# Performance work log

Measured on AMD Instinct MI355X. Metric: run time of the kernel, lower is better.

Reference implementation:

```python
import jax, jax.numpy as jnp
import numpy as np

D_MODEL = 1024
N_HEADS = 16
D_HEAD = D_MODEL // N_HEADS
QLEN = 512
MLEN = 512
BATCH = 8


def setup_inputs() -> dict:
    key = jax.random.key(0)
    ks = jax.random.split(key, 12)
    s = 0.02
    inputs = jax.random.normal(ks[0], (QLEN, BATCH, D_MODEL), jnp.float32)
    r = jax.random.normal(ks[1], (QLEN + MLEN, 1, D_MODEL), jnp.float32)
    u = jax.random.normal(ks[2], (N_HEADS, D_HEAD), jnp.float32) * s
    v = jax.random.normal(ks[3], (N_HEADS, D_HEAD), jnp.float32) * s
    mem = jax.random.normal(ks[4], (MLEN, BATCH, D_MODEL), jnp.float32)
    # attention params (Transformer-XL style): fused qkv, r-projection, output proj
    W_qkv = jax.random.normal(ks[5], (D_MODEL, 3 * D_MODEL), jnp.float32) * s
    W_r = jax.random.normal(ks[6], (D_MODEL, D_MODEL), jnp.float32) * s
    W_o = jax.random.normal(ks[7], (D_MODEL, D_MODEL), jnp.float32) * s
    # GRU params: input-hidden and hidden-hidden for gates (r, z, n), torch layout
    W_ih = jax.random.normal(ks[8], (3 * D_MODEL, D_MODEL), jnp.float32) * s
    W_hh = jax.random.normal(ks[9], (3 * D_MODEL, D_MODEL), jnp.float32) * s
    b_ih = jax.random.normal(ks[10], (3 * D_MODEL,), jnp.float32) * s
    b_hh = jax.random.normal(ks[11], (3 * D_MODEL,), jnp.float32) * s
    h0 = jnp.zeros((BATCH, D_MODEL), jnp.float32)
    return dict(inputs=inputs, r=r, u=u, v=v, mem=mem, W_qkv=W_qkv, W_r=W_r,
                W_o=W_o, W_ih=W_ih, W_hh=W_hh, b_ih=b_ih, b_hh=b_hh, h0=h0)


def _rel_shift(x):
    # x: [q, k, b, h] -> Transformer-XL relative shift
    q, k, b, h = x.shape
    zero_pad = jnp.zeros((q, 1, b, h), x.dtype)
    x_padded = jnp.concatenate([zero_pad, x], axis=1)        # [q, k+1, b, h]
    x_padded = x_padded.reshape(k + 1, q, b, h)
    return x_padded[1:].reshape(q, k, b, h)


def _attention(inputs, r, u, v, mem, W_qkv, W_r, W_o):
    qlen, bsz, _ = inputs.shape
    cat = jnp.concatenate([mem, inputs], axis=0)             # [klen, b, d]
    klen = cat.shape[0]
    qkv = cat @ W_qkv                                        # [klen, b, 3d]
    w_head_q, w_head_k, w_head_v = jnp.split(qkv, 3, axis=-1)
    w_head_q = w_head_q[-qlen:]                              # [q, b, d]
    r_head_k = (r[:, 0, :] @ W_r).reshape(klen, N_HEADS, D_HEAD)  # [k, h, dh]

    q_ = w_head_q.reshape(qlen, bsz, N_HEADS, D_HEAD)
    k_ = w_head_k.reshape(klen, bsz, N_HEADS, D_HEAD)
    v_ = w_head_v.reshape(klen, bsz, N_HEADS, D_HEAD)

    AC = jnp.einsum('ibhd,jbhd->ijbh', q_ + u[None, None], k_)
    BD = jnp.einsum('ibhd,jhd->ijbh', q_ + v[None, None], r_head_k)
    BD = _rel_shift(BD)
    scale = 1.0 / np.sqrt(D_HEAD)
    attn_score = (AC + BD) * scale                           # [q, k, b, h]

    # causal mask with memory: query i attends to keys j <= i + mlen
    mlen = klen - qlen
    i = jnp.arange(qlen)[:, None]
    j = jnp.arange(klen)[None, :]
    mask = j > (i + mlen)                                    # [q, k]
    attn_score = jnp.where(mask[:, :, None, None], -jnp.inf, attn_score)

    attn_prob = jax.nn.softmax(attn_score, axis=1)
    attn_vec = jnp.einsum('ijbh,jbhd->ibhd', attn_prob, v_)
    attn_vec = attn_vec.reshape(qlen, bsz, D_MODEL)
    return attn_vec @ W_o                                    # [q, b, d]


def _gru(x, h0, W_ih, W_hh, b_ih, b_hh):
    # x: [T, B, D]; torch GRU cell math
    Wi_r, Wi_z, Wi_n = jnp.split(W_ih, 3, axis=0)
    Wh_r, Wh_z, Wh_n = jnp.split(W_hh, 3, axis=0)
    bi_r, bi_z, bi_n = jnp.split(b_ih, 3)
    bh_r, bh_z, bh_n = jnp.split(b_hh, 3)

    # precompute input projections for all timesteps
    xr = x @ Wi_r.T + bi_r
    xz = x @ Wi_z.T + bi_z
    xn = x @ Wi_n.T + bi_n

    def step(h, xs):
        xr_t, xz_t, xn_t = xs
        r = jax.nn.sigmoid(xr_t + h @ Wh_r.T + bh_r)
        z = jax.nn.sigmoid(xz_t + h @ Wh_z.T + bh_z)
        n = jnp.tanh(xn_t + r * (h @ Wh_n.T + bh_n))
        h_new = (1.0 - z) * n + z * h
        return h_new, h_new

    _, ys = jax.lax.scan(step, h0, (xr, xz, xn))
    return ys                                                # [T, B, D]


def reference(inputs, r, u, v, mem, W_qkv, W_r, W_o, W_ih, W_hh, b_ih, b_hh, h0):
    y = _attention(inputs, r, u, v, mem, W_qkv, W_r, W_o)
    return _gru(y, h0, W_ih, W_hh, b_ih, b_hh)
```

## Files before the change

kernel.cpp:

```cpp
#include <hip/hip_runtime.h>
#include <math.h>


typedef short bf16x8 __attribute__((ext_vector_type(8)));
typedef float f32x4 __attribute__((ext_vector_type(4)));

union FragU { uint4 u; bf16x8 h; };

__device__ inline void split2(float x0, float x1, unsigned& hi, unsigned& lo) {
    unsigned u0 = __float_as_uint(x0), u1 = __float_as_uint(x1);
    float h0 = __uint_as_float(u0 & 0xffff0000u);
    float h1 = __uint_as_float(u1 & 0xffff0000u);
    unsigned l0 = __float_as_uint(x0 - h0), l1 = __float_as_uint(x1 - h1);
    hi = (u0 >> 16) | (u1 & 0xffff0000u);
    lo = (l0 >> 16) | (l1 & 0xffff0000u);
}

__device__ __forceinline__ unsigned long long ld_coh64(const void* p) {
    return __hip_atomic_load((const unsigned long long*)p, __ATOMIC_RELAXED,
                             __HIP_MEMORY_SCOPE_AGENT);
}
__device__ __forceinline__ void st_coh64(void* p, unsigned long long v) {
    __hip_atomic_store((unsigned long long*)p, v, __ATOMIC_RELAXED,
                       __HIP_MEMORY_SCOPE_AGENT);
}

template<bool TR>
__global__ __launch_bounds__(256) void prep_w(
    const float* __restrict__ W, unsigned* __restrict__ out, int Nr, int K, int ldw)
{
    int idx = blockIdx.x * 256 + threadIdx.x;
    int cpr = K >> 3;
    if (idx >= Nr * cpr) return;
    int n, c;
    if (TR) { n = idx % Nr; c = idx / Nr; }
    else    { c = idx % cpr; n = idx / cpr; }
    int kt = c >> 2, j = c & 3;
    int k = kt * 32 + j * 8;
    float x[8];
    #pragma unroll
    for (int i = 0; i < 8; ++i)
        x[i] = TR ? W[(size_t)(k + i) * ldw + n] : W[(size_t)n * ldw + k + i];
    unsigned h[4], l[4];
    split2(x[0], x[1], h[0], l[0]);
    split2(x[2], x[3], h[1], l[1]);
    split2(x[4], x[5], h[2], l[2]);
    split2(x[6], x[7], h[3], l[3]);
    unsigned* base = out + (size_t)n * K + kt * 32;
    *(uint4*)(base + (((2 * j) ^ (n & 7)) * 4))     = make_uint4(h[0], h[1], h[2], h[3]);
    *(uint4*)(base + (((2 * j + 1) ^ (n & 7)) * 4)) = make_uint4(l[0], l[1], l[2], l[3]);
}

template<int AMODE, bool BIAS>
__global__ __launch_bounds__(256) void gemm_mfma(
    const float* __restrict__ A, const float* __restrict__ A2,
    const unsigned* __restrict__ Bp, const float* __restrict__ bias,
    float* __restrict__ C, int M, int N, int K, int lda, int ldc)
{
    __shared__ uint4 Ab[1024];
    __shared__ uint4 Bb[1024];
    int tid = threadIdx.x;
    int lane = tid & 63, wid = tid >> 6;
    int wr = wid >> 1, wc = wid & 1;
    int n0 = blockIdx.x * 128, m0 = blockIdx.y * 128;
    int r15 = lane & 15, s = lane >> 4;

    f32x4 acc[4][4];
    #pragma unroll
    for (int i = 0; i < 4; ++i)
        #pragma unroll
        for (int j = 0; j < 4; ++j) acc[i][j] = 0.0f;

    for (int kt = 0; kt < (K >> 5); ++kt) {
        int k0 = kt * 32;
        #pragma unroll
        for (int q = 0; q < 2; ++q) {
            int idx = q * 256 + tid;
            int row = idx >> 2, j = idx & 3;
            const float* ap;
            if (AMODE == 1) {
                int gm = m0 + row;
                ap = (gm < 4096) ? (A + (size_t)gm * lda) : (A2 + (size_t)(gm - 4096) * lda);
            } else {
                ap = A + (size_t)(m0 + row) * lda;
            }
            float4 x0 = *(const float4*)(ap + k0 + j * 8);
            float4 x1 = *(const float4*)(ap + k0 + j * 8 + 4);
            unsigned h[4], l[4];
            split2(x0.x, x0.y, h[0], l[0]);
            split2(x0.z, x0.w, h[1], l[1]);
            split2(x1.x, x1.y, h[2], l[2]);
            split2(x1.z, x1.w, h[3], l[3]);
            Ab[row * 8 + (((2 * j) ^ (row & 7)))]     = make_uint4(h[0], h[1], h[2], h[3]);
            Ab[row * 8 + (((2 * j + 1) ^ (row & 7)))] = make_uint4(l[0], l[1], l[2], l[3]);
        }
        #pragma unroll
        for (int q = 0; q < 4; ++q) {
            int idx = q * 256 + tid;
            int row = idx >> 3, slot = idx & 7;
            Bb[idx] = *(const uint4*)(Bp + (size_t)(n0 + row) * K + k0 + slot * 4);
        }
        __syncthreads();
        FragU ahi[4], alo[4], bhi[4], blo[4];
        #pragma unroll
        for (int f = 0; f < 4; ++f) {
            int ar = wr * 64 + f * 16 + r15;
            ahi[f].u = Ab[ar * 8 + ((2 * s) ^ (ar & 7))];
            alo[f].u = Ab[ar * 8 + ((2 * s + 1) ^ (ar & 7))];
            int br = wc * 64 + f * 16 + r15;
            bhi[f].u = Bb[br * 8 + ((2 * s) ^ (br & 7))];
            blo[f].u = Bb[br * 8 + ((2 * s + 1) ^ (br & 7))];
        }
        #pragma unroll
        for (int fi = 0; fi < 4; ++fi)
            #pragma unroll
            for (int fj = 0; fj < 4; ++fj) {
                acc[fi][fj] = __builtin_amdgcn_mfma_f32_16x16x32_bf16(ahi[fi].h, bhi[fj].h, acc[fi][fj], 0, 0, 0);
                acc[fi][fj] = __builtin_amdgcn_mfma_f32_16x16x32_bf16(ahi[fi].h, blo[fj].h, acc[fi][fj], 0, 0, 0);
                acc[fi][fj] = __builtin_amdgcn_mfma_f32_16x16x32_bf16(alo[fi].h, bhi[fj].h, acc[fi][fj], 0, 0, 0);
            }
        __syncthreads();
    }
    int r4 = (lane >> 4) * 4;
    #pragma unroll
    for (int fj = 0; fj < 4; ++fj) {
        int n = n0 + wc * 64 + fj * 16 + r15;
        float bv = BIAS ? bias[n] : 0.f;
        #pragma unroll
        for (int fi = 0; fi < 4; ++fi) {
            int m = m0 + wr * 64 + fi * 16 + r4;
            #pragma unroll
            for (int r = 0; r < 4; ++r)
                C[(size_t)(m + r) * ldc + n] = acc[fi][fj][r] + bv;
        }
    }
}

__global__ __launch_bounds__(256) void attn_fused(
    const float* __restrict__ qkv, const float* __restrict__ rk,
    const float* __restrict__ u_, const float* __restrict__ v_,
    float* __restrict__ y1)
{
    __shared__ float qu[64][68], qv[64][68], Kt[64][68], Vt[64][68];
    __shared__ float RKs[128][68];
    __shared__ float S[64][68];
    __shared__ float mrow[64], lrow[64], scalef[64];
    __shared__ float pmax[64][16], psum[64][16];

    int tid = threadIdx.x;
    int it = blockIdx.x, b = blockIdx.y, h = blockIdx.z;
    int i0 = it * 64;
    int ti = tid >> 4, tj = tid & 15;

    {
        int r = tid >> 2, c0 = (tid & 3) * 16;
        size_t base = ((size_t)(i0 + r + 512) * 8 + b) * 3072 + h * 64;
        #pragma unroll
        for (int q = 0; q < 4; ++q) {
            int c = c0 + q * 4;
            float4 qq = *(const float4*)&qkv[base + c];
            float4 uu = *(const float4*)&u_[h * 64 + c];
            float4 vv = *(const float4*)&v_[h * 64 + c];
            *(float4*)&qu[r][c] = make_float4(qq.x + uu.x, qq.y + uu.y, qq.z + uu.z, qq.w + uu.w);
            *(float4*)&qv[r][c] = make_float4(qq.x + vv.x, qq.y + vv.y, qq.z + vv.z, qq.w + vv.w);
        }
    }
    if (tid < 64) { mrow[tid] = -1e30f; lrow[tid] = 0.f; }

    float Od[4][4] = {};
    int njt = it + 9;

    for (int jt = 0; jt < njt; ++jt) {
        int j0 = jt * 64;
        __syncthreads();
        {
            int r = tid >> 2, c0 = (tid & 3) * 16;
            size_t kb = ((size_t)(j0 + r) * 8 + b) * 3072 + 1024 + h * 64;
            #pragma unroll
            for (int q = 0; q < 4; ++q) {
                int c = c0 + q * 4;
                *(float4*)&Kt[r][c] = *(const float4*)&qkv[kb + c];
                *(float4*)&Vt[r][c] = *(const float4*)&qkv[kb + 1024 + c];
            }
        }
        {
            int r2 = tid >> 1, c0 = (tid & 1) * 32;
            int jj = j0 - i0 + 448 + r2;
            jj = jj < 0 ? 0 : (jj > 1023 ? 1023 : jj);
            size_t rb = (size_t)jj * 1024 + h * 64;
            #pragma unroll
            for (int q = 0; q < 8; ++q) {
                int c = c0 + q * 4;
                *(float4*)&RKs[r2][c] = *(const float4*)&rk[rb + c];
            }
        }
        __syncthreads();

        float acc[4][4] = {};
        int jlb = (tj - ti) * 4 + 60;
        #pragma unroll 4
        for (int d4 = 0; d4 < 64; d4 += 4) {
            float4 Aq[4], Cq[4], Kv[4], Rv[7];
            #pragma unroll
            for (int i = 0; i < 4; ++i) {
                Aq[i] = *(float4*)&qu[ti * 4 + i][d4];
                Cq[i] = *(float4*)&qv[ti * 4 + i][d4];
                Kv[i] = *(float4*)&Kt[tj * 4 + i][d4];
            }
            #pragma unroll
            for (int t = 0; t < 7; ++t)
                Rv[t] = *(float4*)&RKs[jlb + t][d4];
            #pragma unroll
            for (int i = 0; i < 4; ++i)
                #pragma unroll
                for (int j = 0; j < 4; ++j) {
                    float4 kk = Kv[j];
                    float4 rr = Rv[j - i + 3];
                    acc[i][j] += Aq[i].x * kk.x + Aq[i].y * kk.y + Aq[i].z * kk.z + Aq[i].w * kk.w
                               + Cq[i].x * rr.x + Cq[i].y * rr.y + Cq[i].z * rr.z + Cq[i].w * rr.w;
                }
        }
        #pragma unroll
        for (int i = 0; i < 4; ++i) {
            int gi = i0 + ti * 4 + i;
            float mx = -1e30f;
            #pragma unroll
            for (int j = 0; j < 4; ++j) {
                int gj = j0 + tj * 4 + j;
                float vS = acc[i][j] * 0.125f;
                if (gj > gi + 512) vS = -1e30f;
                acc[i][j] = vS;
                mx = fmaxf(mx, vS);
            }
            pmax[ti * 4 + i][tj] = mx;
        }
        __syncthreads();
        if (tid < 64) {
            float mo = mrow[tid], mn = mo;
            #pragma unroll
            for (int t = 0; t < 16; ++t) mn = fmaxf(mn, pmax[tid][t]);
            mrow[tid] = mn;
            scalef[tid] = __expf(mo - mn);
        }
        __syncthreads();
        #pragma unroll
        for (int i = 0; i < 4; ++i) {
            int ri = ti * 4 + i;
            float mn = mrow[ri];
            float4 pv;
            pv.x = __expf(acc[i][0] - mn);
            pv.y = __expf(acc[i][1] - mn);
            pv.z = __expf(acc[i][2] - mn);
            pv.w = __expf(acc[i][3] - mn);
            *(float4*)&S[ri][tj * 4] = pv;
            psum[ri][tj] = pv.x + pv.y + pv.z + pv.w;
            float scl = scalef[ri];
            #pragma unroll
            for (int j2 = 0; j2 < 4; ++j2) Od[i][j2] *= scl;
        }
        __syncthreads();
        if (tid < 64) {
            float s = 0.f;
            #pragma unroll
            for (int t = 0; t < 16; ++t) s += psum[tid][t];
            lrow[tid] = lrow[tid] * scalef[tid] + s;
        }
        #pragma unroll 4
        for (int jb = 0; jb < 64; jb += 4) {
            float4 p0 = *(float4*)&S[ti * 4 + 0][jb];
            float4 p1 = *(float4*)&S[ti * 4 + 1][jb];
            float4 p2 = *(float4*)&S[ti * 4 + 2][jb];
            float4 p3 = *(float4*)&S[ti * 4 + 3][jb];
            float4 v0 = *(float4*)&Vt[jb + 0][tj * 4];
            float4 v1 = *(float4*)&Vt[jb + 1][tj * 4];
            float4 v2 = *(float4*)&Vt[jb + 2][tj * 4];
            float4 v3 = *(float4*)&Vt[jb + 3][tj * 4];
            float4 pr[4] = {p0, p1, p2, p3};
            #pragma unroll
            for (int i = 0; i < 4; ++i) {
                Od[i][0] += pr[i].x * v0.x + pr[i].y * v1.x + pr[i].z * v2.x + pr[i].w * v3.x;
                Od[i][1] += pr[i].x * v0.y + pr[i].y * v1.y + pr[i].z * v2.y + pr[i].w * v3.y;
                Od[i][2] += pr[i].x * v0.z + pr[i].y * v1.z + pr[i].z * v2.z + pr[i].w * v3.z;
                Od[i][3] += pr[i].x * v0.w + pr[i].y * v1.w + pr[i].z * v2.w + pr[i].w * v3.w;
            }
        }
    }
    __syncthreads();
    #pragma unroll
    for (int i = 0; i < 4; ++i) {
        int ri = ti * 4 + i;
        float inv = 1.f / lrow[ri];
        float4 o = make_float4(Od[i][0] * inv, Od[i][1] * inv, Od[i][2] * inv, Od[i][3] * inv);
        *(float4*)&y1[((size_t)(i0 + ri) * 8 + b) * 1024 + h * 64 + tj * 4] = o;
    }
}

__global__ __launch_bounds__(256) void prep_whh(
    const float* __restrict__ Whh, uint4* __restrict__ outp)
{
    int idx = blockIdx.x * 256 + threadIdx.x;
    if (idx >= 393216) return;
    int lane = idx & 63;
    int rest = idx >> 6;
    int gate = rest % 3;
    int kt   = (rest / 3) & 31;
    int g64  = rest / 96;
    int n = gate * 1024 + g64 * 16 + (lane & 15);
    int k = kt * 32 + (lane >> 4) * 8;
    const float* src = Whh + (size_t)n * 1024 + k;
    float4 x0 = *(const float4*)src, x1 = *(const float4*)(src + 4);
    unsigned h[4], l[4];
    split2(x0.x, x0.y, h[0], l[0]);
    split2(x0.z, x0.w, h[1], l[1]);
    split2(x1.x, x1.y, h[2], l[2]);
    split2(x1.z, x1.w, h[3], l[3]);
    outp[((size_t)rest * 2 + 0) * 64 + lane] = make_uint4(h[0], h[1], h[2], h[3]);
    outp[((size_t)rest * 2 + 1) * 64 + lane] = make_uint4(l[0], l[1], l[2], l[3]);
}

__global__ __launch_bounds__(256, 1) void gru_persist2(
    const float* __restrict__ h0, float* __restrict__ hA, float* __restrict__ hB,
    const uint4* __restrict__ WhhG, const float* __restrict__ bhh,
    const float* __restrict__ xg, float* __restrict__ out,
    unsigned* __restrict__ flags)
{
    __shared__ uint4 Bf[4096];
    __shared__ float red[3][64][4];
    int tid = threadIdx.x;
    int lane = tid & 63, wv = tid >> 6;
    int g64 = blockIdx.x;

    int col = lane & 15;
    int d0 = g64 * 16 + (lane >> 4) * 4;
    bool act = (wv == 0) && (col < 8);
    float4 br4 = make_float4(0, 0, 0, 0), bz4 = br4, bn4 = br4;
    if (act) {
        br4 = *(const float4*)&bhh[d0];
        bz4 = *(const float4*)&bhh[1024 + d0];
        bn4 = *(const float4*)&bhh[2048 + d0];
    }
    const uint4* wb = WhhG + (size_t)g64 * 12288 + (wv < 3 ? wv : 0) * 128 + lane;

    for (int t = 0; t < 512; ++t) {
        const float* hi_ = (t == 0) ? h0 : ((t & 1) ? hA : hB);
        float* ho = (t & 1) ? hB : hA;

        float4 xr4, xz4, xn4;
        unsigned long long hp01 = 0, hp23 = 0;
        if (act) {
            size_t xb = ((size_t)t * 8 + col) * 3072 + d0;
            xr4 = *(const float4*)&xg[xb];
            xz4 = *(const float4*)&xg[xb + 1024];
            xn4 = *(const float4*)&xg[xb + 2048];
            hp01 = ld_coh64(hi_ + col * 1024 + d0);
            hp23 = ld_coh64(hi_ + col * 1024 + d0 + 2);
        }

        uint4 wA[16], wB[16];
        #pragma unroll
        for (int q = 0; q < 8; ++q) {
            wA[2 * q]     = wb[q * 384];
            wA[2 * q + 1] = wb[q * 384 + 64];
        }

        unsigned long long hq[16];
        #pragma unroll
        for (int i = 0; i < 4; ++i) {
            int s = i * 256 + tid;
            const float* hp = hi_ + (s & 7) * 1024 + (s >> 5) * 32 + ((s >> 3) & 3) * 8;
            #pragma unroll
            for (int q = 0; q < 4; ++q) hq[i * 4 + q] = ld_coh64(hp + q * 2);
        }
        #pragma unroll
        for (int i = 0; i < 4; ++i) {
            int s = i * 256 + tid;
            int b = s & 7, oct = (s >> 3) & 3, kt = s >> 5;
            float x[8];
            #pragma unroll
            for (int q = 0; q < 4; ++q) {
                x[2 * q]     = __uint_as_float((unsigned)(hq[i * 4 + q] & 0xffffffffu));
                x[2 * q + 1] = __uint_as_float((unsigned)(hq[i * 4 + q] >> 32));
            }
            unsigned hh[4], ll[4];
            split2(x[0], x[1], hh[0], ll[0]);
            split2(x[2], x[3], hh[1], ll[1]);
            split2(x[4], x[5], hh[2], ll[2]);
            split2(x[6], x[7], hh[3], ll[3]);
            int ln = oct * 16 + b;
            Bf[(kt * 2 + 0) * 64 + ln] = make_uint4(hh[0], hh[1], hh[2], hh[3]);
            Bf[(kt * 2 + 1) * 64 + ln] = make_uint4(ll[0], ll[1], ll[2], ll[3]);
        }
        __syncthreads();

        f32x4 acc = 0.0f;
        #define GRU_LOAD(dst, c0)                                   \
            _Pragma("unroll")                                       \
            for (int q = 0; q < 8; ++q) {                           \
                dst[2 * q]     = wb[((c0) * 8 + q) * 384];          \
                dst[2 * q + 1] = wb[((c0) * 8 + q) * 384 + 64];     \
            }
        #define GRU_COMP(src, c0)                                   \
            _Pragma("unroll")                                       \
            for (int q = 0; q < 8; ++q) {                           \
                int kt = (c0) * 8 + q;                              \
                FragU ah, al, bh, bl;                               \
                ah.u = src[2 * q]; al.u = src[2 * q + 1];           \
                bh.u = Bf[(kt * 2 + 0) * 64 + lane];                \
                bl.u = Bf[(kt * 2 + 1) * 64 + lane];                \
                acc = __builtin_amdgcn_mfma_f32_16x16x32_bf16(ah.h, bh.h, acc, 0, 0, 0); \
                acc = __builtin_amdgcn_mfma_f32_16x16x32_bf16(ah.h, bl.h, acc, 0, 0, 0); \
                acc = __builtin_amdgcn_mfma_f32_16x16x32_bf16(al.h, bh.h, acc, 0, 0, 0); \
            }
        if (wv < 3) {
            GRU_LOAD(wB, 1);
            GRU_COMP(wA, 0);
            GRU_LOAD(wA, 2);
            GRU_COMP(wB, 1);
            GRU_LOAD(wB, 3);
            GRU_COMP(wA, 2);
            GRU_COMP(wB, 3);
            *(f32x4*)&red[wv][lane][0] = acc;
        }
        #undef GRU_LOAD
        #undef GRU_COMP
        __syncthreads();

        if (act) {
            f32x4 aR = *(f32x4*)&red[0][lane][0];
            f32x4 aZ = *(f32x4*)&red[1][lane][0];
            f32x4 aN = *(f32x4*)&red[2][lane][0];
            float xr[4] = {xr4.x, xr4.y, xr4.z, xr4.w};
            float xz[4] = {xz4.x, xz4.y, xz4.z, xz4.w};
            float xn[4] = {xn4.x, xn4.y, xn4.z, xn4.w};
            float hp[4] = {__uint_as_float((unsigned)(hp01 & 0xffffffffu)),
                           __uint_as_float((unsigned)(hp01 >> 32)),
                           __uint_as_float((unsigned)(hp23 & 0xffffffffu)),
                           __uint_as_float((unsigned)(hp23 >> 32))};
            float br[4] = {br4.x, br4.y, br4.z, br4.w};
            float bz[4] = {bz4.x, bz4.y, bz4.z, bz4.w};
            float bn[4] = {bn4.x, bn4.y, bn4.z, bn4.w};
            float hn[4];
            #pragma unroll
            for (int r = 0; r < 4; ++r) {
                float rr = 1.f / (1.f + __expf(-(xr[r] + aR[r] + br[r])));
                float zz = 1.f / (1.f + __expf(-(xz[r] + aZ[r] + bz[r])));
                float nn = tanhf(xn[r] + rr * (aN[r] + bn[r]));
                hn[r] = (1.f - zz) * nn + zz * hp[r];
            }
            unsigned long long v01 = (unsigned long long)__float_as_uint(hn[0])
                                   | ((unsigned long long)__float_as_uint(hn[1]) << 32);
            unsigned long long v23 = (unsigned long long)__float_as_uint(hn[2])
                                   | ((unsigned long long)__float_as_uint(hn[3]) << 32);
            st_coh64(ho + col * 1024 + d0, v01);
            st_coh64(ho + col * 1024 + d0 + 2, v23);
            *(float4*)&out[((size_t)t * 8 + col) * 1024 + d0] =
                make_float4(hn[0], hn[1], hn[2], hn[3]);
        }

        if (t != 511) {
            __syncthreads();
            unsigned tgt = (unsigned)t + 1u;
            if (tid < 64) {
                if (tid == 0)
                    __hip_atomic_store(&flags[(size_t)g64 * 16], tgt,
                                       __ATOMIC_RELAXED, __HIP_MEMORY_SCOPE_AGENT);
                const unsigned* fp = &flags[(size_t)tid * 16];
                for (;;) {
                    unsigned f = __hip_atomic_load(fp, __ATOMIC_RELAXED,
                                                   __HIP_MEMORY_SCOPE_AGENT);
                    if (__all(f >= tgt)) break;
                }
            }
            __syncthreads();
        }
    }
}

__global__ __launch_bounds__(192, 1) void gru_step_mfma(
    const float* __restrict__ hin, float* __restrict__ hout,
    const uint4* __restrict__ WhhG, const float* __restrict__ bhh,
    const float* __restrict__ xg, float* __restrict__ out, int t)
{
    __shared__ uint4 Bf[4096];
    __shared__ float red[3][64][4];
    int tid = threadIdx.x;
    int lane = tid & 63, wv = tid >> 6;
    int g64 = blockIdx.x;

    int col = lane & 15;
    int d0 = g64 * 16 + (lane >> 4) * 4;
    bool act = (wv == 0) && (col < 8);
    float4 xr4, xz4, xn4, hp4, br4, bz4, bn4;
    if (act) {
        size_t xb = ((size_t)t * 8 + col) * 3072 + d0;
        xr4 = *(const float4*)&xg[xb];
        xz4 = *(const float4*)&xg[xb + 1024];
        xn4 = *(const float4*)&xg[xb + 2048];
        hp4 = *(const float4*)&hin[col * 1024 + d0];
        br4 = *(const float4*)&bhh[d0];
        bz4 = *(const float4*)&bhh[1024 + d0];
        bn4 = *(const float4*)&bhh[2048 + d0];
    }

    const uint4* wb = WhhG + (size_t)g64 * 12288 + wv * 128 + lane;
    uint4 wA[16], wB[16];
    #pragma unroll
// ... 66 lines not shown
            float rr = 1.f / (1.f + __expf(-(xr[r] + aR[r] + br[r])));
            float zz = 1.f / (1.f + __expf(-(xz[r] + aZ[r] + bz[r])));
            float nn = tanhf(xn[r] + rr * (aN[r] + bn[r]));
            hn[r] = (1.f - zz) * nn + zz * hp[r];
        }
        float4 hv = make_float4(hn[0], hn[1], hn[2], hn[3]);
        *(float4*)&hout[col * 1024 + d0] = hv;
        *(float4*)&out[((size_t)t * 8 + col) * 1024 + d0] = hv;
    }
}

extern "C" void kernel_launch(void* const* d_in, const int* in_sizes, int n_in,
                              void* d_out, int out_size, void* d_ws, size_t ws_size,
                              hipStream_t stream) {
    (void)in_sizes; (void)n_in; (void)out_size; (void)ws_size;
    const float* inputs = (const float*)d_in[0];
    const float* r_in   = (const float*)d_in[1];
    const float* u_in   = (const float*)d_in[2];
    const float* v_in   = (const float*)d_in[3];
    const float* mem    = (const float*)d_in[4];
    const float* Wqkv   = (const float*)d_in[5];
    const float* Wr     = (const float*)d_in[6];
    const float* Wo     = (const float*)d_in[7];
    const float* Wih    = (const float*)d_in[8];
    const float* Whh    = (const float*)d_in[9];
    const float* bih    = (const float*)d_in[10];
    const float* bhh    = (const float*)d_in[11];
    const float* h0     = (const float*)d_in[12];
    float* out = (float*)d_out;
    float* ws = (float*)d_ws;

    float*    qkv   = ws;
    float*    rk    = ws + 25165824;
    float*    y1    = ws + 26214400;
    float*    y2    = ws + 30408704;
    float*    xg    = ws + 34603008;
    float*    hA    = ws + 47185920;
    float*    hB    = ws + 47194112;
    unsigned* WqkvP = (unsigned*)(ws + 47202304);
    unsigned* WrP   = (unsigned*)(ws + 50348032);
    unsigned* WoP   = (unsigned*)(ws + 51396608);
    unsigned* WihP  = (unsigned*)(ws + 52445184);
    unsigned* flags = (unsigned*)(ws + 55590912);
    uint4*    WhhG  = (uint4*)qkv;

    dim3 blk(256);
    prep_w<true ><<<1536, blk, 0, stream>>>(Wqkv, WqkvP, 3072, 1024, 3072);
    prep_w<true ><<< 512, blk, 0, stream>>>(Wr,   WrP,   1024, 1024, 1024);
    prep_w<true ><<< 512, blk, 0, stream>>>(Wo,   WoP,   1024, 1024, 1024);
    prep_w<false><<<1536, blk, 0, stream>>>(Wih,  WihP,  3072, 1024, 1024);
    hipMemsetAsync(flags, 0, 4096, stream);

    gemm_mfma<1, false><<<dim3(24, 64), blk, 0, stream>>>(
        mem, inputs, WqkvP, nullptr, qkv, 8192, 3072, 1024, 1024, 3072);
    gemm_mfma<0, false><<<dim3(8, 8), blk, 0, stream>>>(
        r_in, nullptr, WrP, nullptr, rk, 1024, 1024, 1024, 1024, 1024);
    attn_fused<<<dim3(8, 8, 16), blk, 0, stream>>>(qkv, rk, u_in, v_in, y1);
    prep_whh<<<1536, blk, 0, stream>>>(Whh, WhhG);
    gemm_mfma<0, false><<<dim3(8, 32), blk, 0, stream>>>(
        y1, nullptr, WoP, nullptr, y2, 4096, 1024, 1024, 1024, 1024);
    gemm_mfma<0, true><<<dim3(24, 32), blk, 0, stream>>>(
        y2, nullptr, WihP, bih, xg, 4096, 3072, 1024, 1024, 3072);

    {
        const float* a0 = h0; float* a1 = hA; float* a2 = hB;
        const uint4* a3 = WhhG; const float* a4 = bhh; const float* a5 = xg;
        float* a6 = out; unsigned* a7 = flags;
        void* args[8] = {&a0, &a1, &a2, &a3, &a4, &a5, &a6, &a7};
        hipError_t e = hipLaunchCooperativeKernel((void*)gru_persist2,
                                                  dim3(64), dim3(256), args, 0, stream);
        if (e != hipSuccess) {
            const float* hin = h0;
            for (int s = 0; s < 512; ++s) {
                float* hp = (s & 1) ? hB : hA;
                gru_step_mfma<<<64, dim3(192), 0, stream>>>(hin, hp, WhhG, bhh, xg, out, s);
                hin = hp;
            }
        }
    }
}
```

Baseline: 4.737 ms.

## Replace global barrier in persistent GRU with per-slice flag waits

The all-block barrier at the end of each GRU timestep is replaced by fine-grained waits: each thread spins only on the flag of the block that produced the h slice it is about to load. The flag is published right after the h store drains (s_waitcnt vmcnt(0)), before the output write. The previous hidden state is kept in registers instead of being reloaded, and the MFMA chain is split into four independent accumulators to shorten the dependency chain. Blocks can now start a step as soon as their inputs are ready, but this relies on relaxed atomics plus a waitcnt for ordering and has more threads spinning on flags.

```diff
diff --git a/kernel.cpp b/kernel.cpp
--- a/kernel.cpp
+++ b/kernel.cpp
@@ -318,7 +318,7 @@
     outp[((size_t)rest * 2 + 1) * 64 + lane] = make_uint4(l[0], l[1], l[2], l[3]);
 }
 
-__global__ __launch_bounds__(256, 1) void gru_persist2(
+__global__ __launch_bounds__(256, 1) void gru_persist3(
     const float* __restrict__ h0, float* __restrict__ hA, float* __restrict__ hB,
     const uint4* __restrict__ WhhG, const float* __restrict__ bhh,
     const float* __restrict__ xg, float* __restrict__ out,
@@ -333,48 +333,62 @@
     int col = lane & 15;
     int d0 = g64 * 16 + (lane >> 4) * 4;
     bool act = (wv == 0) && (col < 8);
-    float4 br4 = make_float4(0, 0, 0, 0), bz4 = br4, bn4 = br4;
+    float4 br4 = make_float4(0, 0, 0, 0), bz4 = br4, bn4 = br4, hprev4 = br4;
     if (act) {
         br4 = *(const float4*)&bhh[d0];
         bz4 = *(const float4*)&bhh[1024 + d0];
         bn4 = *(const float4*)&bhh[2048 + d0];
+        hprev4 = *(const float4*)&h0[col * 1024 + d0];
     }
     const uint4* wb = WhhG + (size_t)g64 * 12288 + (wv < 3 ? wv : 0) * 128 + lane;
+
+    int toff[4], tkt[4], tln[4];
+    const unsigned* tfl[4];
+    #pragma unroll
+    for (int i = 0; i < 4; ++i) {
+        int s = i * 256 + tid;
+        int b = s & 7, oct = (s >> 3) & 3, kt = s >> 5;
+        toff[i] = b * 1024 + kt * 32 + oct * 8;
+        tkt[i] = kt;
+        tln[i] = oct * 16 + b;
+        tfl[i] = &flags[(size_t)(2 * kt + (oct >> 1)) * 16];
+    }
 
     for (int t = 0; t < 512; ++t) {
         const float* hi_ = (t == 0) ? h0 : ((t & 1) ? hA : hB);
         float* ho = (t & 1) ? hB : hA;
 
         float4 xr4, xz4, xn4;
-        unsigned long long hp01 = 0, hp23 = 0;
         if (act) {
             size_t xb = ((size_t)t * 8 + col) * 3072 + d0;
             xr4 = *(const float4*)&xg[xb];
             xz4 = *(const float4*)&xg[xb + 1024];
             xn4 = *(const float4*)&xg[xb + 2048];
-            hp01 = ld_coh64(hi_ + col * 1024 + d0);
-            hp23 = ld_coh64(hi_ + col * 1024 + d0 + 2);
         }
 
         uint4 wA[16], wB[16];
-        #pragma unroll
-        for (int q = 0; q < 8; ++q) {
-            wA[2 * q]     = wb[q * 384];
-            wA[2 * q + 1] = wb[q * 384 + 64];
+        if (wv < 3) {
+            #pragma unroll
+            for (int q = 0; q < 8; ++q) {
+                wA[2 * q]     = wb[q * 384];
+                wA[2 * q + 1] = wb[q * 384 + 64];
+            }
         }
 
         unsigned long long hq[16];
+        unsigned tgt = (unsigned)t;
         #pragma unroll
         for (int i = 0; i < 4; ++i) {
-            int s = i * 256 + tid;
-            const float* hp = hi_ + (s & 7) * 1024 + (s >> 5) * 32 + ((s >> 3) & 3) * 8;
+            if (t > 0) {
+                while (__hip_atomic_load(tfl[i], __ATOMIC_RELAXED,
+                                         __HIP_MEMORY_SCOPE_AGENT) < tgt) {}
+            }
+            const float* hp = hi_ + toff[i];
             #pragma unroll
             for (int q = 0; q < 4; ++q) hq[i * 4 + q] = ld_coh64(hp + q * 2);
         }
         #pragma unroll
         for (int i = 0; i < 4; ++i) {
-            int s = i * 256 + tid;
-            int b = s & 7, oct = (s >> 3) & 3, kt = s >> 5;
             float x[8];
             #pragma unroll
             for (int q = 0; q < 4; ++q) {
@@ -386,20 +400,18 @@
             split2(x[2], x[3], hh[1], ll[1]);
             split2(x[4], x[5], hh[2], ll[2]);
             split2(x[6], x[7], hh[3], ll[3]);
-            int ln = oct * 16 + b;
-            Bf[(kt * 2 + 0) * 64 + ln] = make_uint4(hh[0], hh[1], hh[2], hh[3]);
-            Bf[(kt * 2 + 1) * 64 + ln] = make_uint4(ll[0], ll[1], ll[2], ll[3]);
-        }
-        __syncthreads();
-
-        f32x4 acc = 0.0f;
+            Bf[(tkt[i] * 2 + 0) * 64 + tln[i]] = make_uint4(hh[0], hh[1], hh[2], hh[3]);
+            Bf[(tkt[i] * 2 + 1) * 64 + tln[i]] = make_uint4(ll[0], ll[1], ll[2], ll[3]);
+        }
+        __syncthreads();
+
         #define GRU_LOAD(dst, c0)                                   \
             _Pragma("unroll")                                       \
             for (int q = 0; q < 8; ++q) {                           \
                 dst[2 * q]     = wb[((c0) * 8 + q) * 384];          \
                 dst[2 * q + 1] = wb[((c0) * 8 + q) * 384 + 64];     \
             }
-        #define GRU_COMP(src, c0)                                   \
+        #define GRU_COMP(src, c0, a)                                \
             _Pragma("unroll")                                       \
             for (int q = 0; q < 8; ++q) {                           \
                 int kt = (c0) * 8 + q;                              \
@@ -407,24 +419,27 @@
                 ah.u = src[2 * q]; al.u = src[2 * q + 1];           \
                 bh.u = Bf[(kt * 2 + 0) * 64 + lane];                \
                 bl.u = Bf[(kt * 2 + 1) * 64 + lane];                \
-                acc = __builtin_amdgcn_mfma_f32_16x16x32_bf16(ah.h, bh.h, acc, 0, 0, 0); \
-                acc = __builtin_amdgcn_mfma_f32_16x16x32_bf16(ah.h, bl.h, acc, 0, 0, 0); \
-                acc = __builtin_amdgcn_mfma_f32_16x16x32_bf16(al.h, bh.h, acc, 0, 0, 0); \
+                a = __builtin_amdgcn_mfma_f32_16x16x32_bf16(ah.h, bh.h, a, 0, 0, 0); \
+                a = __builtin_amdgcn_mfma_f32_16x16x32_bf16(ah.h, bl.h, a, 0, 0, 0); \
+                a = __builtin_amdgcn_mfma_f32_16x16x32_bf16(al.h, bh.h, a, 0, 0, 0); \
             }
         if (wv < 3) {
+            f32x4 a0 = 0.0f, a1 = 0.0f, a2 = 0.0f, a3 = 0.0f;
             GRU_LOAD(wB, 1);
-            GRU_COMP(wA, 0);
+            GRU_COMP(wA, 0, a0);
             GRU_LOAD(wA, 2);
-            GRU_COMP(wB, 1);
+            GRU_COMP(wB, 1, a1);
             GRU_LOAD(wB, 3);
-            GRU_COMP(wA, 2);
-            GRU_COMP(wB, 3);
-            *(f32x4*)&red[wv][lane][0] = acc;
+            GRU_COMP(wA, 2, a2);
+            GRU_COMP(wB, 3, a3);
+            f32x4 av = (a0 + a1) + (a2 + a3);
+            *(f32x4*)&red[wv][lane][0] = av;
         }
         #undef GRU_LOAD
         #undef GRU_COMP
         __syncthreads();
 
+        float hn[4];
         if (act) {
             f32x4 aR = *(f32x4*)&red[0][lane][0];
             f32x4 aZ = *(f32x4*)&red[1][lane][0];
@@ -432,14 +447,10 @@
             float xr[4] = {xr4.x, xr4.y, xr4.z, xr4.w};
             float xz[4] = {xz4.x, xz4.y, xz4.z, xz4.w};
             float xn[4] = {xn4.x, xn4.y, xn4.z, xn4.w};
-            float hp[4] = {__uint_as_float((unsigned)(hp01 & 0xffffffffu)),
-                           __uint_as_float((unsigned)(hp01 >> 32)),
-                           __uint_as_float((unsigned)(hp23 & 0xffffffffu)),
-                           __uint_as_float((unsigned)(hp23 >> 32))};
+            float hp[4] = {hprev4.x, hprev4.y, hprev4.z, hprev4.w};
             float br[4] = {br4.x, br4.y, br4.z, br4.w};
             float bz[4] = {bz4.x, bz4.y, bz4.z, bz4.w};
             float bn[4] = {bn4.x, bn4.y, bn4.z, bn4.w};
-            float hn[4];
             #pragma unroll
             for (int r = 0; r < 4; ++r) {
                 float rr = 1.f / (1.f + __expf(-(xr[r] + aR[r] + br[r])));
@@ -453,25 +464,18 @@
                                    | ((unsigned long long)__float_as_uint(hn[3]) << 32);
             st_coh64(ho + col * 1024 + d0, v01);
             st_coh64(ho + col * 1024 + d0 + 2, v23);
+        }
+        if (wv == 0) {
+            asm volatile("s_waitcnt vmcnt(0)" ::: "memory");
+            __builtin_amdgcn_sched_barrier(0);
+            if (tid == 0 && t != 511)
+                __hip_atomic_store(&flags[(size_t)g64 * 16], (unsigned)(t + 1),
+                                   __ATOMIC_RELAXED, __HIP_MEMORY_SCOPE_AGENT);
+        }
+        if (act) {
             *(float4*)&out[((size_t)t * 8 + col) * 1024 + d0] =
                 make_float4(hn[0], hn[1], hn[2], hn[3]);
-        }
-
-        if (t != 511) {
-            __syncthreads();
-            unsigned tgt = (unsigned)t + 1u;
-            if (tid < 64) {
-                if (tid == 0)
-                    __hip_atomic_store(&flags[(size_t)g64 * 16], tgt,
-                                       __ATOMIC_RELAXED, __HIP_MEMORY_SCOPE_AGENT);
-                const unsigned* fp = &flags[(size_t)tid * 16];
-                for (;;) {
-                    unsigned f = __hip_atomic_load(fp, __ATOMIC_RELAXED,
-                                                   __HIP_MEMORY_SCOPE_AGENT);
-                    if (__all(f >= tgt)) break;
-                }
-            }
-            __syncthreads();
+            hprev4 = make_float4(hn[0], hn[1], hn[2], hn[3]);
         }
     }
 }
@@ -639,7 +643,7 @@
         const uint4* a3 = WhhG; const float* a4 = bhh; const float* a5 = xg;
         float* a6 = out; unsigned* a7 = flags;
         void* args[8] = {&a0, &a1, &a2, &a3, &a4, &a5, &a6, &a7};
-        hipError_t e = hipLaunchCooperativeKernel((void*)gru_persist2,
+        hipError_t e = hipLaunchCooperativeKernel((void*)gru_persist3,
                                                   dim3(64), dim3(256), args, 0, stream);
         if (e != hipSuccess) {
             const float* hin = h0;
```

Measured after the change: 4.827 ms. No clear change (+1.9%).

## Pre-split GEMM A operands to bf16 hi/lo layout and load via global_load_lds

Applied to the files above, without the earlier changes.

Adds a prep pass that splits the concatenated mem/inputs, y1 and y2 activations into swizzled bf16 hi/lo packed layout. A new gemm_pp kernel then streams both A and B tiles straight into LDS with global_load_lds instead of converting fp32 inside the GEMM. This removes the per-tile split work and register staging from the GEMM inner loop. In exchange it adds extra prep kernels and global traffic, and reuses workspace regions (qkv, xg) as scratch, which relies on their lifetimes not overlapping.

```diff
diff --git a/kernel.cpp b/kernel.cpp
--- a/kernel.cpp
+++ b/kernel.cpp
@@ -23,6 +23,12 @@
 __device__ __forceinline__ void st_coh64(void* p, unsigned long long v) {
     __hip_atomic_store((unsigned long long*)p, v, __ATOMIC_RELAXED,
                        __HIP_MEMORY_SCOPE_AGENT);
+}
+
+__device__ __forceinline__ void gl_lds16(const uint4* g, uint4* l) {
+    __builtin_amdgcn_global_load_lds(
+        (const __attribute__((address_space(1))) uint4*)g,
+        (__attribute__((address_space(3))) uint4*)l, 16, 0, 0);
 }
 
 template<bool TR>
@@ -51,6 +57,93 @@
     *(uint4*)(base + (((2 * j + 1) ^ (n & 7)) * 4)) = make_uint4(l[0], l[1], l[2], l[3]);
 }
 
+__global__ __launch_bounds__(256) void prep_cat(
+    const float* __restrict__ mem, const float* __restrict__ inputs,
+    unsigned* __restrict__ out)
+{
+    int idx = blockIdx.x * 256 + threadIdx.x;
+    if (idx >= 1048576) return;
+    int c = idx & 127, n = idx >> 7;
+    int kt = c >> 2, j = c & 3;
+    int k = kt * 32 + j * 8;
+    const float* src = (n < 4096) ? (mem + (size_t)n * 1024 + k)
+                                  : (inputs + (size_t)(n - 4096) * 1024 + k);
+    float4 x0 = *(const float4*)src, x1 = *(const float4*)(src + 4);
+    unsigned h[4], l[4];
+    split2(x0.x, x0.y, h[0], l[0]);
+    split2(x0.z, x0.w, h[1], l[1]);
+    split2(x1.x, x1.y, h[2], l[2]);
+    split2(x1.z, x1.w, h[3], l[3]);
+    unsigned* base = out + (size_t)n * 1024 + kt * 32;
+    *(uint4*)(base + (((2 * j) ^ (n & 7)) * 4))     = make_uint4(h[0], h[1], h[2], h[3]);
+    *(uint4*)(base + (((2 * j + 1) ^ (n & 7)) * 4)) = make_uint4(l[0], l[1], l[2], l[3]);
+}
+
+template<bool BIAS>
+__global__ __launch_bounds__(256) void gemm_pp(
+    const uint4* __restrict__ Ap4, const uint4* __restrict__ Bp4,
+    const float* __restrict__ bias, float* __restrict__ C, int K, int ldc)
+{
+    __shared__ uint4 Ab[1024];
+    __shared__ uint4 Bb[1024];
+    int tid = threadIdx.x;
+    int lane = tid & 63, wid = tid >> 6;
+    int wr = wid >> 1, wc = wid & 1;
+    int n0 = blockIdx.x * 128, m0 = blockIdx.y * 128;
+    int r15 = lane & 15, s = lane >> 4;
+    int K4 = K >> 2;
+
+    f32x4 acc[4][4];
+    #pragma unroll
+    for (int i = 0; i < 4; ++i)
+        #pragma unroll
+        for (int j = 0; j < 4; ++j) acc[i][j] = 0.0f;
+
+    for (int kt = 0; kt < (K >> 5); ++kt) {
+        #pragma unroll
+        for (int q = 0; q < 4; ++q) {
+            int base = q * 256 + wid * 64;
+            int idx  = base + lane;
+            int row = idx >> 3, slot = idx & 7;
+            gl_lds16(Ap4 + (size_t)(m0 + row) * K4 + kt * 8 + slot, &Ab[base]);
+            gl_lds16(Bp4 + (size_t)(n0 + row) * K4 + kt * 8 + slot, &Bb[base]);
+        }
+        __syncthreads();
+        FragU ahi[4], alo[4], bhi[4], blo[4];
+        #pragma unroll
+        for (int f = 0; f < 4; ++f) {
+            int ar = wr * 64 + f * 16 + r15;
+            ahi[f].u = Ab[ar * 8 + ((2 * s) ^ (ar & 7))];
+            alo[f].u = Ab[ar * 8 + ((2 * s + 1) ^ (ar & 7))];
+            int br = wc * 64 + f * 16 + r15;
+            bhi[f].u = Bb[br * 8 + ((2 * s) ^ (br & 7))];
+            blo[f].u = Bb[br * 8 + ((2 * s + 1) ^ (br & 7))];
+        }
+        #pragma unroll
+        for (int fi = 0; fi < 4; ++fi)
+            #pragma unroll
+            for (int fj = 0; fj < 4; ++fj) {
+                acc[fi][fj] = __builtin_amdgcn_mfma_f32_16x16x32_bf16(ahi[fi].h, bhi[fj].h, acc[fi][fj], 0, 0, 0);
+                acc[fi][fj] = __builtin_amdgcn_mfma_f32_16x16x32_bf16(ahi[fi].h, blo[fj].h, acc[fi][fj], 0, 0, 0);
+                acc[fi][fj] = __builtin_amdgcn_mfma_f32_16x16x32_bf16(alo[fi].h, bhi[fj].h, acc[fi][fj], 0, 0, 0);
+            }
+        __syncthreads();
+    }
+    int r4 = (lane >> 4) * 4;
+    #pragma unroll
+    for (int fj = 0; fj < 4; ++fj) {
+        int n = n0 + wc * 64 + fj * 16 + r15;
+        float bv = BIAS ? bias[n] : 0.f;
+        #pragma unroll
+        for (int fi = 0; fi < 4; ++fi) {
+            int m = m0 + wr * 64 + fi * 16 + r4;
+            #pragma unroll
+            for (int r = 0; r < 4; ++r)
+                C[(size_t)(m + r) * ldc + n] = acc[fi][fj][r] + bv;
+        }
+    }
+}
+
 template<int AMODE, bool BIAS>
 __global__ __launch_bounds__(256) void gemm_mfma(
     const float* __restrict__ A, const float* __restrict__ A2,
@@ -615,6 +708,9 @@
     unsigned* WihP  = (unsigned*)(ws + 52445184);
     unsigned* flags = (unsigned*)(ws + 55590912);
     uint4*    WhhG  = (uint4*)qkv;
+    unsigned* y1P   = (unsigned*)(qkv + 4194304);
+    unsigned* y2P   = (unsigned*)(qkv + 8388608);
+    unsigned* catP  = (unsigned*)xg;
 
     dim3 blk(256);
     prep_w<true ><<<1536, blk, 0, stream>>>(Wqkv, WqkvP, 3072, 1024, 3072);
@@ -623,16 +719,19 @@
     prep_w<false><<<1536, blk, 0, stream>>>(Wih,  WihP,  3072, 1024, 1024);
     hipMemsetAsync(flags, 0, 4096, stream);
 
-    gemm_mfma<1, false><<<dim3(24, 64), blk, 0, stream>>>(
-        mem, inputs, WqkvP, nullptr, qkv, 8192, 3072, 1024, 1024, 3072);
+    prep_cat<<<4096, blk, 0, stream>>>(mem, inputs, catP);
+    gemm_pp<false><<<dim3(24, 64), blk, 0, stream>>>(
+        (const uint4*)catP, (const uint4*)WqkvP, nullptr, qkv, 1024, 3072);
     gemm_mfma<0, false><<<dim3(8, 8), blk, 0, stream>>>(
         r_in, nullptr, WrP, nullptr, rk, 1024, 1024, 1024, 1024, 1024);
     attn_fused<<<dim3(8, 8, 16), blk, 0, stream>>>(qkv, rk, u_in, v_in, y1);
     prep_whh<<<1536, blk, 0, stream>>>(Whh, WhhG);
-    gemm_mfma<0, false><<<dim3(8, 32), blk, 0, stream>>>(
-        y1, nullptr, WoP, nullptr, y2, 4096, 1024, 1024, 1024, 1024);
-    gemm_mfma<0, true><<<dim3(24, 32), blk, 0, stream>>>(
-        y2, nullptr, WihP, bih, xg, 4096, 3072, 1024, 1024, 3072);
+    prep_w<false><<<2048, blk, 0, stream>>>(y1, y1P, 4096, 1024, 1024);
+    gemm_pp<false><<<dim3(8, 32), blk, 0, stream>>>(
+        (const uint4*)y1P, (const uint4*)WoP, nullptr, y2, 1024, 1024);
+    prep_w<false><<<2048, blk, 0, stream>>>(y2, y2P, 4096, 1024, 1024);
+    gemm_pp<true><<<dim3(24, 32), blk, 0, stream>>>(
+        (const uint4*)y2P, (const uint4*)WihP, bih, xg, 1024, 3072);
 
     {
         const float* a0 = h0; float* a1 = hA; float* a2 = hB;
```

Result: no change. 4.719 ms (-0.4%).

## Pre-split GEMM operands to bf16 hi/lo and load tiles via global_load_lds

Applied to the files above, without the earlier changes.

Merges all weight and activation preparation into one prep_all kernel that writes operands in the swizzled bf16 hi/lo layout. The GEMMs then stream both A and B tiles straight into LDS with global_load_lds instead of splitting A inside the inner loop. The QKV GEMM skips the Q columns for memory rows, since only the last qlen rows of Q are used. The attention and W_o GEMM epilogues now emit the split-packed layout for the next GEMM. Attention softmax row max and sum move from shared-memory reductions with barriers to wave shuffles. The cost is more kernels writing packed intermediates and reuse of the xg buffer as scratch.

```diff
diff --git a/kernel.cpp b/kernel.cpp
--- a/kernel.cpp
+++ b/kernel.cpp
@@ -25,22 +25,15 @@
                        __HIP_MEMORY_SCOPE_AGENT);
 }
 
-template<bool TR>
-__global__ __launch_bounds__(256) void prep_w(
-    const float* __restrict__ W, unsigned* __restrict__ out, int Nr, int K, int ldw)
+__device__ __forceinline__ void gl_lds16(const uint4* g, uint4* l) {
+    __builtin_amdgcn_global_load_lds(
+        (const __attribute__((address_space(1))) uint4*)g,
+        (__attribute__((address_space(3))) uint4*)l, 16, 0, 0);
+}
+
+__device__ __forceinline__ void split_store8(
+    const float* x, unsigned* out, int n, int K, int kt, int j)
 {
-    int idx = blockIdx.x * 256 + threadIdx.x;
-    int cpr = K >> 3;
-    if (idx >= Nr * cpr) return;
-    int n, c;
-    if (TR) { n = idx % Nr; c = idx / Nr; }
-    else    { c = idx % cpr; n = idx / cpr; }
-    int kt = c >> 2, j = c & 3;
-    int k = kt * 32 + j * 8;
-    float x[8];
-    #pragma unroll
-    for (int i = 0; i < 8; ++i)
-        x[i] = TR ? W[(size_t)(k + i) * ldw + n] : W[(size_t)n * ldw + k + i];
     unsigned h[4], l[4];
     split2(x[0], x[1], h[0], l[0]);
     split2(x[2], x[3], h[1], l[1]);
@@ -51,19 +44,72 @@
     *(uint4*)(base + (((2 * j + 1) ^ (n & 7)) * 4)) = make_uint4(l[0], l[1], l[2], l[3]);
 }
 
-template<int AMODE, bool BIAS>
-__global__ __launch_bounds__(256) void gemm_mfma(
-    const float* __restrict__ A, const float* __restrict__ A2,
-    const unsigned* __restrict__ Bp, const float* __restrict__ bias,
-    float* __restrict__ C, int M, int N, int K, int lda, int ldc)
+#define SEG0 1048576
+#define SEG1 1441792
+#define SEG2 1572864
+#define SEG3 1703936
+#define SEG4 2097152
+#define SEG5 2228224
+
+__global__ __launch_bounds__(256) void prep_all(
+    const float* __restrict__ mem, const float* __restrict__ inputs,
+    const float* __restrict__ Wqkv, const float* __restrict__ Wr,
+    const float* __restrict__ Wo, const float* __restrict__ Wih,
+    const float* __restrict__ r_in,
+    unsigned* __restrict__ catP, unsigned* __restrict__ WqkvP,
+    unsigned* __restrict__ WrP, unsigned* __restrict__ WoP,
+    unsigned* __restrict__ WihP, unsigned* __restrict__ rP)
 {
-    __shared__ uint4 Ab[1024];
-    __shared__ uint4 Bb[1024];
+    int idx = blockIdx.x * 256 + threadIdx.x;
+    if (idx >= SEG5) return;
+    float x[8];
+    if (idx < SEG0) {
+        int c = idx & 127, n = idx >> 7;
+        int kt = c >> 2, j = c & 3, k = kt * 32 + j * 8;
+        const float* src = (n < 4096) ? (mem + (size_t)n * 1024 + k)
+                                      : (inputs + (size_t)(n - 4096) * 1024 + k);
+        float4 a = *(const float4*)src, b = *(const float4*)(src + 4);
+        x[0]=a.x; x[1]=a.y; x[2]=a.z; x[3]=a.w; x[4]=b.x; x[5]=b.y; x[6]=b.z; x[7]=b.w;
+        split_store8(x, catP, n, 1024, kt, j);
+    } else if (idx < SEG3) {
+        int i, Nr, ldw; const float* W; unsigned* out;
+        if (idx < SEG1)      { i = idx - SEG0; Nr = 3072; ldw = 3072; W = Wqkv; out = WqkvP; }
+        else if (idx < SEG2) { i = idx - SEG1; Nr = 1024; ldw = 1024; W = Wr;   out = WrP;  }
+        else                 { i = idx - SEG2; Nr = 1024; ldw = 1024; W = Wo;   out = WoP;  }
+        int n = i % Nr, c = i / Nr;
+        int kt = c >> 2, j = c & 3, k = kt * 32 + j * 8;
+        #pragma unroll
+        for (int q = 0; q < 8; ++q) x[q] = W[(size_t)(k + q) * ldw + n];
+        split_store8(x, out, n, 1024, kt, j);
+    } else {
+        int i; const float* W; unsigned* out;
+        if (idx < SEG4) { i = idx - SEG3; W = Wih;  out = WihP; }
+        else            { i = idx - SEG4; W = r_in; out = rP;   }
+        int c = i & 127, n = i >> 7;
+        int kt = c >> 2, j = c & 3, k = kt * 32 + j * 8;
+        float4 a = *(const float4*)(W + (size_t)n * 1024 + k);
+        float4 b = *(const float4*)(W + (size_t)n * 1024 + k + 4);
+        x[0]=a.x; x[1]=a.y; x[2]=a.z; x[3]=a.w; x[4]=b.x; x[5]=b.y; x[6]=b.z; x[7]=b.w;
+        split_store8(x, out, n, 1024, kt, j);
+    }
+}
+
+template<bool BIAS, bool SPLITOUT>
+__global__ __launch_bounds__(256) void gemm_pp(
+    const uint4* __restrict__ Ap4, const uint4* __restrict__ Bp4,
+    const float* __restrict__ bias, float* __restrict__ C,
+    unsigned* __restrict__ Cp, int K, int ldc)
+{
+    __shared__ uint4 SH[2048];
+    uint4* Ab = SH;
+    uint4* Bb = SH + 1024;
     int tid = threadIdx.x;
     int lane = tid & 63, wid = tid >> 6;
     int wr = wid >> 1, wc = wid & 1;
     int n0 = blockIdx.x * 128, m0 = blockIdx.y * 128;
     int r15 = lane & 15, s = lane >> 4;
+    int r4 = (lane >> 4) * 4;
+    int K4 = K >> 2;
 
     f32x4 acc[4][4];
     #pragma unroll
@@ -72,33 +118,13 @@
         for (int j = 0; j < 4; ++j) acc[i][j] = 0.0f;
 
     for (int kt = 0; kt < (K >> 5); ++kt) {
-        int k0 = kt * 32;
-        #pragma unroll
-        for (int q = 0; q < 2; ++q) {
-            int idx = q * 256 + tid;
-            int row = idx >> 2, j = idx & 3;
-            const float* ap;
-            if (AMODE == 1) {
-                int gm = m0 + row;
-                ap = (gm < 4096) ? (A + (size_t)gm * lda) : (A2 + (size_t)(gm - 4096) * lda);
-            } else {
-                ap = A + (size_t)(m0 + row) * lda;
-            }
-            float4 x0 = *(const float4*)(ap + k0 + j * 8);
-            float4 x1 = *(const float4*)(ap + k0 + j * 8 + 4);
-            unsigned h[4], l[4];
-            split2(x0.x, x0.y, h[0], l[0]);
-            split2(x0.z, x0.w, h[1], l[1]);
-            split2(x1.x, x1.y, h[2], l[2]);
-            split2(x1.z, x1.w, h[3], l[3]);
-            Ab[row * 8 + (((2 * j) ^ (row & 7)))]     = make_uint4(h[0], h[1], h[2], h[3]);
-            Ab[row * 8 + (((2 * j + 1) ^ (row & 7)))] = make_uint4(l[0], l[1], l[2], l[3]);
-        }
         #pragma unroll
         for (int q = 0; q < 4; ++q) {
-            int idx = q * 256 + tid;
+            int base = q * 256 + wid * 64;
+            int idx  = base + lane;
             int row = idx >> 3, slot = idx & 7;
-            Bb[idx] = *(const uint4*)(Bp + (size_t)(n0 + row) * K + k0 + slot * 4);
+            gl_lds16(Ap4 + (size_t)(m0 + row) * K4 + kt * 8 + slot, &Ab[base]);
+            gl_lds16(Bp4 + (size_t)(n0 + row) * K4 + kt * 8 + slot, &Bb[base]);
         }
         __syncthreads();
         FragU ahi[4], alo[4], bhi[4], blo[4];
@@ -121,17 +147,46 @@
             }
         __syncthreads();
     }
-    int r4 = (lane >> 4) * 4;
-    #pragma unroll
-    for (int fj = 0; fj < 4; ++fj) {
-        int n = n0 + wc * 64 + fj * 16 + r15;
-        float bv = BIAS ? bias[n] : 0.f;
-        #pragma unroll
-        for (int fi = 0; fi < 4; ++fi) {
-            int m = m0 + wr * 64 + fi * 16 + r4;
-            #pragma unroll
-            for (int r = 0; r < 4; ++r)
-                C[(size_t)(m + r) * ldc + n] = acc[fi][fj][r] + bv;
+
+    if (!SPLITOUT) {
+        #pragma unroll
+        for (int fj = 0; fj < 4; ++fj) {
+            int n = n0 + wc * 64 + fj * 16 + r15;
+            float bv = BIAS ? bias[n] : 0.f;
+            #pragma unroll
+            for (int fi = 0; fi < 4; ++fi) {
+                int m = m0 + wr * 64 + fi * 16 + r4;
+                #pragma unroll
+                for (int r = 0; r < 4; ++r)
+                    C[(size_t)(m + r) * ldc + n] = acc[fi][fj][r] + bv;
+            }
+        }
+    } else {
+        float* Cs = (float*)SH;
+        #pragma unroll
+        for (int half = 0; half < 2; ++half) {
+            __syncthreads();
+            if (wr == half) {
+                #pragma unroll
+                for (int fi = 0; fi < 4; ++fi)
+                    #pragma unroll
+                    for (int fj = 0; fj < 4; ++fj)
+                        #pragma unroll
+                        for (int r = 0; r < 4; ++r)
+                            Cs[(fi * 16 + r4 + r) * 128 + wc * 64 + fj * 16 + r15] = acc[fi][fj][r];
+            }
+            __syncthreads();
+            #pragma unroll
+            for (int q = 0; q < 4; ++q) {
+                int oc = q * 256 + tid;
+                int lr = oc >> 4, oct = oc & 15;
+                float x[8];
+                *(float4*)&x[0] = *(float4*)&Cs[lr * 128 + oct * 8];
+                *(float4*)&x[4] = *(float4*)&Cs[lr * 128 + oct * 8 + 4];
+                int m = m0 + half * 64 + lr;
+                int k = n0 + oct * 8;
+                split_store8(x, Cp, m, ldc, k >> 5, (k >> 3) & 3);
+            }
         }
     }
 }
@@ -139,13 +194,11 @@
 __global__ __launch_bounds__(256) void attn_fused(
     const float* __restrict__ qkv, const float* __restrict__ rk,
     const float* __restrict__ u_, const float* __restrict__ v_,
-    float* __restrict__ y1)
+    unsigned* __restrict__ y1P)
 {
     __shared__ float qu[64][68], qv[64][68], Kt[64][68], Vt[64][68];
     __shared__ float RKs[128][68];
     __shared__ float S[64][68];
-    __shared__ float mrow[64], lrow[64], scalef[64];
-    __shared__ float pmax[64][16], psum[64][16];
 
     int tid = threadIdx.x;
     int it = blockIdx.x, b = blockIdx.y, h = blockIdx.z;
@@ -165,8 +218,9 @@
             *(float4*)&qv[r][c] = make_float4(qq.x + vv.x, qq.y + vv.y, qq.z + vv.z, qq.w + vv.w);
         }
     }
-    if (tid < 64) { mrow[tid] = -1e30f; lrow[tid] = 0.f; }
-
+
+    float m[4] = {-1e30f, -1e30f, -1e30f, -1e30f};
+    float l[4] = {0.f, 0.f, 0.f, 0.f};
     float Od[4][4] = {};
     int njt = it + 9;
 
@@ -232,39 +286,29 @@
                 acc[i][j] = vS;
                 mx = fmaxf(mx, vS);
             }
-            pmax[ti * 4 + i][tj] = mx;
-        }
-        __syncthreads();
-        if (tid < 64) {
-            float mo = mrow[tid], mn = mo;
-            #pragma unroll
-            for (int t = 0; t < 16; ++t) mn = fmaxf(mn, pmax[tid][t]);
-            mrow[tid] = mn;
-            scalef[tid] = __expf(mo - mn);
-        }
-        __syncthreads();
-        #pragma unroll
-        for (int i = 0; i < 4; ++i) {
-            int ri = ti * 4 + i;
-            float mn = mrow[ri];
+            mx = fmaxf(mx, __shfl_xor(mx, 1));
+            mx = fmaxf(mx, __shfl_xor(mx, 2));
+            mx = fmaxf(mx, __shfl_xor(mx, 4));
+            mx = fmaxf(mx, __shfl_xor(mx, 8));
+            float mn = fmaxf(m[i], mx);
+            float sc = __expf(m[i] - mn);
+            m[i] = mn;
             float4 pv;
             pv.x = __expf(acc[i][0] - mn);
             pv.y = __expf(acc[i][1] - mn);
             pv.z = __expf(acc[i][2] - mn);
             pv.w = __expf(acc[i][3] - mn);
-            *(float4*)&S[ri][tj * 4] = pv;
-            psum[ri][tj] = pv.x + pv.y + pv.z + pv.w;
-            float scl = scalef[ri];
-            #pragma unroll
-            for (int j2 = 0; j2 < 4; ++j2) Od[i][j2] *= scl;
-        }
-        __syncthreads();
-        if (tid < 64) {
-            float s = 0.f;
-            #pragma unroll
-            for (int t = 0; t < 16; ++t) s += psum[tid][t];
-            lrow[tid] = lrow[tid] * scalef[tid] + s;
-        }
+            *(float4*)&S[ti * 4 + i][tj * 4] = pv;
+            float ps = pv.x + pv.y + pv.z + pv.w;
+            ps += __shfl_xor(ps, 1);
+            ps += __shfl_xor(ps, 2);
+            ps += __shfl_xor(ps, 4);
+            ps += __shfl_xor(ps, 8);
+            l[i] = l[i] * sc + ps;
+            #pragma unroll
+            for (int j2 = 0; j2 < 4; ++j2) Od[i][j2] *= sc;
+        }
+        asm volatile("" ::: "memory");
         #pragma unroll 4
         for (int jb = 0; jb < 64; jb += 4) {
             float4 p0 = *(float4*)&S[ti * 4 + 0][jb];
@@ -285,13 +329,21 @@
             }
         }
     }
-    __syncthreads();
     #pragma unroll
     for (int i = 0; i < 4; ++i) {
         int ri = ti * 4 + i;
-        float inv = 1.f / lrow[ri];
+        float inv = 1.f / l[i];
         float4 o = make_float4(Od[i][0] * inv, Od[i][1] * inv, Od[i][2] * inv, Od[i][3] * inv);
-        *(float4*)&y1[((size_t)(i0 + ri) * 8 + b) * 1024 + h * 64 + tj * 4] = o;
+        int n = (i0 + ri) * 8 + b;
+        unsigned hw0, hw1, lw0, lw1;
+        split2(o.x, o.y, hw0, lw0);
+        split2(o.z, o.w, hw1, lw1);
+        int kt2 = 2 * h + (tj >> 3);
+        int j2 = (tj >> 1) & 3;
+        int wo = (tj & 1) * 2;
+        unsigned* bp = y1P + (size_t)n * 1024 + kt2 * 32;
+        *(uint2*)(bp + (((2 * j2)     ^ (n & 7)) * 4) + wo) = make_uint2(hw0, hw1);
+        *(uint2*)(bp + (((2 * j2 + 1) ^ (n & 7)) * 4) + wo) = make_uint2(lw0, lw1);
     }
 }
 
@@ -604,8 +656,8 @@
 
     float*    qkv   = ws;
     float*    rk    = ws + 25165824;
-    float*    y1    = ws + 26214400;
-    float*    y2    = ws + 30408704;
+    unsigned* y1P   = (unsigned*)(ws + 26214400);
+    unsigned* y2P   = (unsigned*)(ws + 30408704);
     float*    xg    = ws + 34603008;
     float*    hA    = ws + 47185920;
     float*    hB    = ws + 47194112;
@@ -615,24 +667,28 @@
     unsigned* WihP  = (unsigned*)(ws + 52445184);
     unsigned* flags = (unsigned*)(ws + 55590912);
     uint4*    WhhG  = (uint4*)qkv;
+    unsigned* catP  = (unsigned*)xg;
+    unsigned* rP    = (unsigned*)xg + 8388608;
 
     dim3 blk(256);
-    prep_w<true ><<<1536, blk, 0, stream>>>(Wqkv, WqkvP, 3072, 1024, 3072);
-    prep_w<true ><<< 512, blk, 0, stream>>>(Wr,   WrP,   1024, 1024, 1024);
-    prep_w<true ><<< 512, blk, 0, stream>>>(Wo,   WoP,   1024, 1024, 1024);
-    prep_w<false><<<1536, blk, 0, stream>>>(Wih,  WihP,  3072, 1024, 1024);
     hipMemsetAsync(flags, 0, 4096, stream);
-
-    gemm_mfma<1, false><<<dim3(24, 64), blk, 0, stream>>>(
-        mem, inputs, WqkvP, nullptr, qkv, 8192, 3072, 1024, 1024, 3072);
-    gemm_mfma<0, false><<<dim3(8, 8), blk, 0, stream>>>(
-        r_in, nullptr, WrP, nullptr, rk, 1024, 1024, 1024, 1024, 1024);
-    attn_fused<<<dim3(8, 8, 16), blk, 0, stream>>>(qkv, rk, u_in, v_in, y1);
+    prep_all<<<8704, blk, 0, stream>>>(mem, inputs, Wqkv, Wr, Wo, Wih, r_in,
+                                       catP, WqkvP, WrP, WoP, WihP, rP);
+
+    gemm_pp<false, false><<<dim3(16, 32), blk, 0, stream>>>(
+        (const uint4*)catP, (const uint4*)WqkvP + 1024 * 256, nullptr,
+        qkv + 1024, nullptr, 1024, 3072);
+    gemm_pp<false, false><<<dim3(24, 32), blk, 0, stream>>>(
+        (const uint4*)catP + 4096 * 256, (const uint4*)WqkvP, nullptr,
+        qkv + (size_t)4096 * 3072, nullptr, 1024, 3072);
+    gemm_pp<false, false><<<dim3(8, 8), blk, 0, stream>>>(
+        (const uint4*)rP, (const uint4*)WrP, nullptr, rk, nullptr, 1024, 1024);
+    attn_fused<<<dim3(8, 8, 16), blk, 0, stream>>>(qkv, rk, u_in, v_in, y1P);
     prep_whh<<<1536, blk, 0, stream>>>(Whh, WhhG);
-    gemm_mfma<0, false><<<dim3(8, 32), blk, 0, stream>>>(
-        y1, nullptr, WoP, nullptr, y2, 4096, 1024, 1024, 1024, 1024);
-    gemm_mfma<0, true><<<dim3(24, 32), blk, 0, stream>>>(
-        y2, nullptr, WihP, bih, xg, 4096, 3072, 1024, 1024, 3072);
+    gemm_pp<false, true><<<dim3(8, 32), blk, 0, stream>>>(
+        (const uint4*)y1P, (const uint4*)WoP, nullptr, nullptr, y2P, 1024, 1024);
+    gemm_pp<true, false><<<dim3(24, 32), blk, 0, stream>>>(
+        (const uint4*)y2P, (const uint4*)WihP, bih, xg, nullptr, 1024, 3072);
 
     {
         const float* a0 = h0; float* a1 = hA; float* a2 = hB;
```

Result: no change. 4.672 ms (-1.4%).
